# Kernel tuning notes

Hardware: AMD Instinct MI355X
Metric: run time of the kernel (lower is better)

## Reference

```python
import jax, jax.numpy as jnp
import numpy as np

D = 1024      # d_model
H = 16        # nhead
DH = D // H   # head_dim = 64
ROT = DH // 2 # rotary_ndims = 32
FFN = 4096    # d_ffn
B, T, M, N = 4, 1024, 128, 64


def _layernorm(x, g, b, eps=1e-5):
    mu = jnp.mean(x, axis=-1, keepdims=True)
    var = jnp.mean(jnp.square(x - mu), axis=-1, keepdims=True)
    return (x - mu) * jax.lax.rsqrt(var + eps) * g + b


def _rotate_half(x):
    x1, x2 = x[..., : x.shape[-1] // 2], x[..., x.shape[-1] // 2:]
    return jnp.concatenate([-x2, x1], axis=-1)


def setup_inputs() -> dict:
    key = jax.random.key(0)
    ks = jax.random.split(key, 16)
    s = 0.02
    inp = {
        'x': jax.random.normal(ks[0], (B, T, D), jnp.float32),
        'memory': jax.random.normal(ks[1], (B, M, D), jnp.float32),
        'nmr': jax.random.normal(ks[2], (B, N, D), jnp.float32),
        'Wq': jax.random.normal(ks[3], (D, D), jnp.float32) * s,
        'bq': jnp.zeros((D,), jnp.float32),
        'Wk': jax.random.normal(ks[4], (D, D), jnp.float32) * s,
        'bk': jnp.zeros((D,), jnp.float32),
        'Wv': jax.random.normal(ks[5], (D, D), jnp.float32) * s,
        'bv': jnp.zeros((D,), jnp.float32),
        'Wo': jax.random.normal(ks[6], (D, D), jnp.float32) * s,
        'bo': jnp.zeros((D,), jnp.float32),
        'W1': jax.random.normal(ks[7], (D, FFN), jnp.float32) * s,
        'b1': jnp.zeros((FFN,), jnp.float32),
        'W2': jax.random.normal(ks[8], (FFN, D), jnp.float32) * s,
        'b2': jnp.zeros((D,), jnp.float32),
        'ln1_g': jnp.ones((D,), jnp.float32),
        'ln1_b': jnp.zeros((D,), jnp.float32),
        'ln2_g': jnp.ones((D,), jnp.float32),
        'ln2_b': jnp.zeros((D,), jnp.float32),
    }
    return inp


def reference(x, memory, nmr, Wq, bq, Wk, bk, Wv, bv, Wo, bo, W1, b1, W2, b2,
              ln1_g, ln1_b, ln2_g, ln2_b):
    b, t, _ = x.shape
    m, n = memory.shape[1], nmr.shape[1]
    pref = m + n
    L = pref + t

    x_full = jnp.concatenate([memory, nmr, x], axis=1)  # (B, L, D)
    xa = _layernorm(x_full, ln1_g, ln1_b)

    def heads(w, bias):
        return (xa @ w + bias).reshape(b, L, H, DH).transpose(0, 2, 1, 3)  # (B,H,L,DH)

    q = heads(Wq, bq)
    k = heads(Wk, bk)
    v = heads(Wv, bv)

    # partial RoPE on first ROT dims of each head
    pos = jnp.arange(L, dtype=jnp.float32)
    inv_freq = 1.0 / (10000.0 ** (jnp.arange(0, ROT, 2, dtype=jnp.float32) / ROT))
    freqs = pos[:, None] * inv_freq[None, :]              # (L, ROT/2)
    emb = jnp.concatenate([freqs, freqs], axis=-1)        # (L, ROT)
    cos, sin = jnp.cos(emb), jnp.sin(emb)
    qr, qp = q[..., :ROT], q[..., ROT:]
    kr, kp = k[..., :ROT], k[..., ROT:]
    qr = qr * cos + _rotate_half(qr) * sin
    kr = kr * cos + _rotate_half(kr) * sin
    q = jnp.concatenate([qr, qp], axis=-1)
    k = jnp.concatenate([kr, kp], axis=-1)

    # block mask: prefix (memory+nmr) fully bidirectional, target causal,
    # target attends to full prefix, prefix does NOT attend to target.
    i = jnp.arange(L)
    allowed = (i[None, :] < pref) | ((i[:, None] >= pref) & (i[None, :] >= pref)
                                     & (i[None, :] <= i[:, None]))  # (L, L)

    scale = 1.0 / jnp.sqrt(jnp.asarray(DH, jnp.float32))
    scores = jnp.einsum('bhqd,bhkd->bhqk', q, k) * scale
    scores = jnp.where(allowed[None, None], scores, jnp.finfo(scores.dtype).min)
    probs = jax.nn.softmax(scores, axis=-1)
    attn = jnp.einsum('bhqk,bhkd->bhqd', probs, v)        # (B,H,L,DH)
    attn = attn.transpose(0, 2, 1, 3).reshape(b, L, D)

    x_full = attn @ Wo + bo + x_full

    xf = _layernorm(x_full, ln2_g, ln2_b)
    xf = jnp.square(jax.nn.relu(xf @ W1 + b1)) @ W2 + b2
    x_full = x_full + xf

    return x_full[:, pref:]
```

## Files before the change

### kernel.cpp

```cpp
#include <hip/hip_runtime.h>
#include <hip/hip_bf16.h>
#include <math.h>

#define D_   1024
#define H_   16
#define DH_  64
#define FFN_ 4096
#define B_   4
#define T_   1024
#define M_   128
#define N_   64
#define PREF 192
#define L_   1216
#define BL_  (B_*L_)
#define BT_  (B_*T_)

typedef __attribute__((ext_vector_type(4))) float f32x4;
typedef __attribute__((ext_vector_type(8))) short bf16x8;
typedef __attribute__((ext_vector_type(8))) unsigned short u16x8;
typedef const __attribute__((address_space(1))) void gvoid_t;
typedef __attribute__((address_space(3))) void lvoid_t;

#define LGKM0 asm volatile("s_waitcnt lgkmcnt(0)" ::: "memory")
#define CFENCE asm volatile("" ::: "memory")

__device__ __forceinline__ void gl_lds16(const void* g, void* l) {
    __builtin_amdgcn_global_load_lds((gvoid_t*)g, (lvoid_t*)l, 16, 0, 0);
}

__device__ __forceinline__ ushort f2bf(float x) {
    union { __hip_bfloat16 h; ushort u; } cv;
    cv.h = __float2bfloat16(x);
    return cv.u;
}

__device__ __forceinline__ u16x8 pack8(float4 a, float4 b) {
    u16x8 r;
    r[0]=f2bf(a.x); r[1]=f2bf(a.y); r[2]=f2bf(a.z); r[3]=f2bf(a.w);
    r[4]=f2bf(b.x); r[5]=f2bf(b.y); r[6]=f2bf(b.z); r[7]=f2bf(b.w);
    return r;
}

__device__ __forceinline__ float block_reduce_sum256(float v, float* sbuf) {
#pragma unroll
    for (int o = 32; o > 0; o >>= 1) v += __shfl_xor(v, o, 64);
    int w = threadIdx.x >> 6;
    if ((threadIdx.x & 63) == 0) sbuf[w] = v;
    __syncthreads();
    float r = sbuf[0] + sbuf[1] + sbuf[2] + sbuf[3];
    __syncthreads();
    return r;
}

__device__ __forceinline__ void wtr_body(const float* __restrict__ W,
                                         ushort* __restrict__ Wt, int K, int Nc)
{
    __shared__ float tl[64][65];
    int c0 = blockIdx.x << 6, k0 = blockIdx.y << 6;
    int tid = threadIdx.x;
    int rr = tid >> 4, c4 = (tid & 15) << 2;
#pragma unroll
    for (int p = 0; p < 4; ++p) {
        int r = (p << 4) + rr;
        float4 v = *(const float4*)(W + (size_t)(k0 + r) * Nc + c0 + c4);
        tl[r][c4+0] = v.x; tl[r][c4+1] = v.y; tl[r][c4+2] = v.z; tl[r][c4+3] = v.w;
    }
    __syncthreads();
#pragma unroll
    for (int p = 0; p < 4; ++p) {
        int rT = (p << 4) + rr;
        ushort4 uv;
        uv.x = f2bf(tl[c4+0][rT]);
        uv.y = f2bf(tl[c4+1][rT]);
        uv.z = f2bf(tl[c4+2][rT]);
        uv.w = f2bf(tl[c4+3][rT]);
        *(ushort4*)(Wt + (size_t)(c0 + rT) * K + k0 + c4) = uv;
    }
}

__global__ __launch_bounds__(256) void wtr_kernel(
    const float* __restrict__ W, ushort* __restrict__ Wt, int K, int Nc)
{ wtr_body(W, Wt, K, Nc); }

__global__ __launch_bounds__(256) void wtr4_kernel(
    const float* __restrict__ W0, const float* __restrict__ W1,
    const float* __restrict__ W2, const float* __restrict__ W3,
    ushort* __restrict__ T0, ushort* __restrict__ T1,
    ushort* __restrict__ T2, ushort* __restrict__ T3)
{
    const float* W; ushort* T;
    switch (blockIdx.z) {
        case 0: W = W0; T = T0; break;
        case 1: W = W1; T = T1; break;
        case 2: W = W2; T = T2; break;
        default: W = W3; T = T3; break;
    }
    wtr_body(W, T, D_, D_);
}

__global__ __launch_bounds__(256) void prep_kernel(
    float* __restrict__ tab, const float* __restrict__ bq,
    const float* __restrict__ bk, const float* __restrict__ bv,
    float* __restrict__ ob)
{
    int i = blockIdx.x * 256 + threadIdx.x;
    if (i < L_ * 32) {
        int pos = i >> 5, idx = i & 31;
        int fi = idx & 15;
        float invf = exp2f(-(float)fi * 0.83048202372f);
        float th = (float)pos * invf;
        tab[i] = (idx < 16) ? cosf(th) : sinf(th);
    } else {
        int j = i - L_ * 32;
        if (j < 3072) {
            float v = (j < 1024) ? bq[j] : (j < 2048 ? bk[j - 1024] : bv[j - 2048]);
            ob[j] = v;
        }
    }
}

__global__ __launch_bounds__(256) void ln1_concat_kernel(
    const float* __restrict__ x, const float* __restrict__ mem,
    const float* __restrict__ nmr, const float* __restrict__ g,
    const float* __restrict__ be, float* __restrict__ x_full,
    ushort* __restrict__ xa_bf)
{
    __shared__ float sbuf[4];
    int row = blockIdx.x;
    int b = row / L_, pos = row % L_;
    const float* src;
    if (pos < M_)          src = mem + ((size_t)b*M_ + pos)      * D_;
    else if (pos < M_+N_)  src = nmr + ((size_t)b*N_ + (pos-M_)) * D_;
    else                   src = x   + ((size_t)b*T_ + (pos-PREF))*D_;

    int c = threadIdx.x << 2;
    float4 v = *(const float4*)(src + c);
    float s = v.x + v.y + v.z + v.w;
    s = block_reduce_sum256(s, sbuf);
    float mu = s * (1.0f / D_);
    float dx = v.x - mu, dy = v.y - mu, dz = v.z - mu, dw = v.w - mu;
    float q = dx*dx + dy*dy + dz*dz + dw*dw;
    q = block_reduce_sum256(q, sbuf);
    float inv = rsqrtf(q * (1.0f / D_) + 1e-5f);
    float4 gv = *(const float4*)(g + c);
    float4 bv = *(const float4*)(be + c);
    ushort4 o;
    o.x = f2bf(dx*inv*gv.x + bv.x);
    o.y = f2bf(dy*inv*gv.y + bv.y);
    o.z = f2bf(dz*inv*gv.z + bv.z);
    o.w = f2bf(dw*inv*gv.w + bv.w);
    *(float4*)(x_full + (size_t)row*D_ + c) = v;
    *(ushort4*)(xa_bf + (size_t)row*D_ + c) = o;
}

__global__ __launch_bounds__(256) void ln2_kernel(
    const float* __restrict__ src, const float* __restrict__ g,
    const float* __restrict__ be, ushort* __restrict__ dst)
{
    __shared__ float sbuf[4];
    int row = blockIdx.x;
    int c = threadIdx.x << 2;
    float4 v = *(const float4*)(src + (size_t)row*D_ + c);
    float s = v.x + v.y + v.z + v.w;
    s = block_reduce_sum256(s, sbuf);
    float mu = s * (1.0f / D_);
    float dx = v.x - mu, dy = v.y - mu, dz = v.z - mu, dw = v.w - mu;
    float q = dx*dx + dy*dy + dz*dz + dw*dw;
    q = block_reduce_sum256(q, sbuf);
    float inv = rsqrtf(q * (1.0f / D_) + 1e-5f);
    float4 gv = *(const float4*)(g + c);
    float4 bv = *(const float4*)(be + c);
    ushort4 o;
    o.x = f2bf(dx*inv*gv.x + bv.x);
    o.y = f2bf(dy*inv*gv.y + bv.y);
    o.z = f2bf(dz*inv*gv.z + bv.z);
    o.w = f2bf(dw*inv*gv.w + bv.w);
    *(ushort4*)(dst + (size_t)row*D_ + c) = o;
}

__global__ __launch_bounds__(256) void gemm_bf16_kernel(
    const ushort* __restrict__ A, const ushort* __restrict__ Bt,
    const float* __restrict__ bias, const float* __restrict__ rtab,
    void* __restrict__ Cout, int Nc, int Kstride, int Klen, int mode)
{
    __shared__ ushort SM[24576];
    char* SMb = (char*)SM;
    int tid = threadIdx.x;
    int lane = tid & 63, w = tid >> 6;
    int wm = w >> 1, wn = w & 1;
    int nx = gridDim.x;
    int flat = blockIdx.y * nx + blockIdx.x;
    int cpx = (nx * gridDim.y) >> 3;
    int sz = (flat & 7) * cpx + (flat >> 3);
    int row0 = (sz / nx) << 7, col0 = (sz % nx) << 7;
    int l15 = lane & 15, l4 = lane >> 4;

    f32x4 acc[4][4] = {};

    int r_a = tid >> 2;
    int sc  = tid & 3;
    int lcOff = (sc ^ ((r_a >> 1) & 3)) << 3;
    const ushort* Arow  = A  + (size_t)(row0 + r_a)      * Kstride;
    const ushort* Arow2 = A  + (size_t)(row0 + 64 + r_a) * Kstride;
    const ushort* Brow  = Bt + (size_t)(col0 + r_a)      * Kstride;
    const ushort* Brow2 = Bt + (size_t)(col0 + 64 + r_a) * Kstride;

#define STAGEQ(bb, k0rel)                                                    \
    do { char* Ab = SMb + (bb)*8192; char* Bb = SMb + 24576 + (bb)*8192;     \
        gl_lds16(Arow  + (k0rel) + lcOff, Ab + (tid << 4));                  \
        gl_lds16(Arow2 + (k0rel) + lcOff, Ab + 4096 + (tid << 4));           \
        gl_lds16(Brow  + (k0rel) + lcOff, Bb + (tid << 4));                  \
        gl_lds16(Brow2 + (k0rel) + lcOff, Bb + 4096 + (tid << 4));           \
    } while (0)

    int nIt = Klen >> 5;
    STAGEQ(0, 0);
    STAGEQ(1, 32);
    int cur = 0;
    for (int it = 0; it < nIt; ++it) {
        if (it + 1 < nIt) {
            asm volatile("s_waitcnt vmcnt(4)" ::: "memory");
        } else {
            asm volatile("s_waitcnt vmcnt(0)" ::: "memory");
        }
        __builtin_amdgcn_s_barrier();
        CFENCE;
        if (it + 2 < nIt) {
            int s2 = cur + 2; if (s2 >= 3) s2 -= 3;
            STAGEQ(s2, (it + 2) << 5);
        }
        const ushort* As = (const ushort*)(SMb + cur*8192);
        const ushort* Bs = (const ushort*)(SMb + 24576 + cur*8192);
        bf16x8 af[4], bfr[4];
#pragma unroll
        for (int i = 0; i < 4; ++i) {
            int ra = (wm << 6) + (i << 4) + l15;
            af[i]  = *(const bf16x8*)(&As[ra*32 + ((l4 ^ ((ra >> 1) & 3)) << 3)]);
            int rb = (wn << 6) + (i << 4) + l15;
            bfr[i] = *(const bf16x8*)(&Bs[rb*32 + ((l4 ^ ((rb >> 1) & 3)) << 3)]);
        }
#pragma unroll
        for (int i = 0; i < 4; ++i)
#pragma unroll
            for (int j = 0; j < 4; ++j)
                acc[i][j] = __builtin_amdgcn_mfma_f32_16x16x32_bf16(af[i], bfr[j], acc[i][j], 0, 0, 0);
        CFENCE;
        cur = (cur + 1 == 3) ? 0 : cur + 1;
    }
#undef STAGEQ
    __syncthreads();

    float bcol[4];
#pragma unroll
    for (int j = 0; j < 4; ++j) bcol[j] = bias[col0 + (wn << 6) + (j << 4) + l15];

    float* scr = (float*)SM + w * 1088;
    int rr = lane >> 2, cseg = lane & 3;
    int hh = ((col0 & 1023) + (wn << 6)) >> 6;
    int which = col0 >> 10;

#pragma unroll
    for (int i = 0; i < 4; ++i) {
        LGKM0;
#pragma unroll
        for (int j = 0; j < 4; ++j)
#pragma unroll
            for (int r = 0; r < 4; ++r)
                scr[((l4 << 2) + r)*68 + (j << 4) + l15] = acc[i][j][r] + bcol[j];
        LGKM0;
        int grow = row0 + (wm << 6) + (i << 4) + rr;

        if (which == 2) {
            int r0g = row0 + (wm << 6) + (i << 4);
            int bb = r0g / L_;
            int posb = r0g - bb * L_;
            float4 v0, v1, v2, v3;
            v0.x = scr[ 0*68 + lane]; v0.y = scr[ 1*68 + lane];
            v0.z = scr[ 2*68 + lane]; v0.w = scr[ 3*68 + lane];
            v1.x = scr[ 4*68 + lane]; v1.y = scr[ 5*68 + lane];
            v1.z = scr[ 6*68 + lane]; v1.w = scr[ 7*68 + lane];
            v2.x = scr[ 8*68 + lane]; v2.y = scr[ 9*68 + lane];
            v2.z = scr[10*68 + lane]; v2.w = scr[11*68 + lane];
            v3.x = scr[12*68 + lane]; v3.y = scr[13*68 + lane];
            v3.z = scr[14*68 + lane]; v3.w = scr[15*68 + lane];
            ushort* O = (ushort*)Cout + 2*(size_t)BL_*D_;
            size_t base = ((size_t)(bb*H_ + hh)*64 + lane)*L_ + posb;
            *(u16x8*)(O + base)     = pack8(v0, v1);
            *(u16x8*)(O + base + 8) = pack8(v2, v3);
        } else {
            int bb = grow / L_;
            int pos = grow - bb * L_;
            float4 a0 = *(float4*)&scr[rr*68 + (cseg << 4) + 0];
            float4 a1 = *(float4*)&scr[rr*68 + (cseg << 4) + 4];
            float4 a2 = *(float4*)&scr[rr*68 + (cseg << 4) + 8];
            float4 a3 = *(float4*)&scr[rr*68 + (cseg << 4) + 12];
            if (cseg < 2) {
                int oseg = cseg ^ 1;
                float4 p0 = *(float4*)&scr[rr*68 + (oseg << 4) + 0];
                float4 p1 = *(float4*)&scr[rr*68 + (oseg << 4) + 4];
                float4 p2 = *(float4*)&scr[rr*68 + (oseg << 4) + 8];
                float4 p3 = *(float4*)&scr[rr*68 + (oseg << 4) + 12];
                const float* tb = rtab + pos*32;
                float4 c0 = *(const float4*)(tb + 0),  c1 = *(const float4*)(tb + 4);
                float4 c2 = *(const float4*)(tb + 8),  c3 = *(const float4*)(tb + 12);
                float4 s0 = *(const float4*)(tb + 16), s1 = *(const float4*)(tb + 20);
                float4 s2 = *(const float4*)(tb + 24), s3 = *(const float4*)(tb + 28);
                float sg = (cseg == 0) ? -1.f : 1.f;
                a0.x = a0.x*c0.x + sg*p0.x*s0.x; a0.y = a0.y*c0.y + sg*p0.y*s0.y;
                a0.z = a0.z*c0.z + sg*p0.z*s0.z; a0.w = a0.w*c0.w + sg*p0.w*s0.w;
                a1.x = a1.x*c1.x + sg*p1.x*s1.x; a1.y = a1.y*c1.y + sg*p1.y*s1.y;
                a1.z = a1.z*c1.z + sg*p1.z*s1.z; a1.w = a1.w*c1.w + sg*p1.w*s1.w;
                a2.x = a2.x*c2.x + sg*p2.x*s2.x; a2.y = a2.y*c2.y + sg*p2.y*s2.y;
                a2.z = a2.z*c2.z + sg*p2.z*s2.z; a2.w = a2.w*c2.w + sg*p2.w*s2.w;
                a3.x = a3.x*c3.x + sg*p3.x*s3.x; a3.y = a3.y*c3.y + sg*p3.y*s3.y;
                a3.z = a3.z*c3.z + sg*p3.z*s3.z; a3.w = a3.w*c3.w + sg*p3.w*s3.w;
            }
            ushort* O = (ushort*)Cout + (size_t)which * ((size_t)BL_*D_);
            size_t base = (((size_t)(bb*H_ + hh)*L_ + pos) << 6) + (cseg << 4);
            *(u16x8*)(O + base)     = pack8(a0, a1);
            *(u16x8*)(O + base + 8) = pack8(a2, a3);
        }
    }
}

__global__ __launch_bounds__(512) void gemm_ffn1_kernel(
    const ushort* __restrict__ A, const ushort* __restrict__ Bt,
    const float* __restrict__ bias, void* __restrict__ Cout,
    int Nc, int Kstride, int Klen)
{
    __shared__ ushort SM[36864];
    char* SMb = (char*)SM;

    int tid = threadIdx.x;
    int lane = tid & 63, w = tid >> 6;
    int l15 = lane & 15, l4 = lane >> 4;

    int nx = gridDim.x;
    int flat = blockIdx.y * nx + blockIdx.x;
    int cpx = (nx * gridDim.y) >> 3;
    int sz = (flat & 7) * cpx + (flat >> 3);
    int row0 = (sz / nx) << 7, col0 = (sz % nx) << 8;

    int wm = w >> 2, wn = w & 3;

    f32x4 acc[4][4] = {};

    int rA = tid >> 2, scA = tid & 3;
    int lcA = (scA ^ ((rA >> 1) & 3)) << 3;
    const ushort* Ar = A + (size_t)(row0 + rA) * Kstride + lcA;
    int lcB1 = (scA ^ (((128 + rA) >> 1) & 3)) << 3;
    const ushort* Br0 = Bt + (size_t)(col0 + rA)       * Kstride + lcA;
    const ushort* Br1 = Bt + (size_t)(col0 + 128 + rA) * Kstride + lcB1;

#define STG1(bb, k0rel)                                                       \
    do {                                                                      \
        gl_lds16(Ar  + (k0rel), SMb + (bb)*8192 + (tid << 4));                \
        gl_lds16(Br0 + (k0rel), SMb + 24576 + (bb)*16384 + (tid << 4));       \
        gl_lds16(Br1 + (k0rel), SMb + 24576 + (bb)*16384 + 8192 + (tid << 4));\
    } while (0)

    int nIt = Klen >> 5;
    STG1(0, 0);
    STG1(1, 32);
    int cur = 0;
    for (int it = 0; it < nIt; ++it) {
        if (it + 1 < nIt) {
            asm volatile("s_waitcnt vmcnt(3)" ::: "memory");
        } else {
            asm volatile("s_waitcnt vmcnt(0)" ::: "memory");
        }
        __builtin_amdgcn_s_barrier();
        CFENCE;
        if (it + 2 < nIt) {
            int s2 = cur + 2; if (s2 >= 3) s2 -= 3;
            STG1(s2, (it + 2) << 5);
        }
        const ushort* As = (const ushort*)(SMb + cur*8192);
        const ushort* Bs = (const ushort*)(SMb + 24576 + cur*16384);
        bf16x8 af[4], bfr[4];
#pragma unroll
        for (int i = 0; i < 4; ++i) {
            int ra = (wm << 6) + (i << 4) + l15;
            af[i]  = *(const bf16x8*)(&As[ra*32 + ((l4 ^ ((ra >> 1) & 3)) << 3)]);
            int rb = (wn << 6) + (i << 4) + l15;
            bfr[i] = *(const bf16x8*)(&Bs[rb*32 + ((l4 ^ ((rb >> 1) & 3)) << 3)]);
        }
#pragma unroll
        for (int i = 0; i < 4; ++i)
#pragma unroll
            for (int j = 0; j < 4; ++j)
                acc[i][j] = __builtin_amdgcn_mfma_f32_16x16x32_bf16(af[i], bfr[j], acc[i][j], 0, 0, 0);
        CFENCE;
        cur = (cur + 1 == 3) ? 0 : cur + 1;
    }
#undef STG1
    __syncthreads();

    float bcol[4];
#pragma unroll
    for (int j = 0; j < 4; ++j) bcol[j] = bias[col0 + (wn << 6) + (j << 4) + l15];

    float* scr = (float*)SMb + w * 1088;
    int rr = lane >> 2, cseg = lane & 3;
    int colbase = col0 + (wn << 6);

#pragma unroll
    for (int i = 0; i < 4; ++i) {
        LGKM0;
#pragma unroll
        for (int j = 0; j < 4; ++j)
#pragma unroll
            for (int r = 0; r < 4; ++r) {
                float v = acc[i][j][r] + bcol[j];
                v = fmaxf(v, 0.f); v *= v;
                scr[((l4 << 2) + r)*68 + (j << 4) + l15] = v;
            }
        LGKM0;
        int grow = row0 + (wm << 6) + (i << 4) + rr;
        float4 q0 = *(float4*)&scr[rr*68 + (cseg << 4) + 0];
        float4 q1 = *(float4*)&scr[rr*68 + (cseg << 4) + 4];
        float4 q2 = *(float4*)&scr[rr*68 + (cseg << 4) + 8];
        float4 q3 = *(float4*)&scr[rr*68 + (cseg << 4) + 12];
        int gcol = colbase + (cseg << 4);
        ushort* O = (ushort*)Cout;
        *(u16x8*)(O + (size_t)grow*Nc + gcol)     = pack8(q0, q1);
        *(u16x8*)(O + (size_t)grow*Nc + gcol + 8) = pack8(q2, q3);
    }
}

__global__ __launch_bounds__(256) void gemm_sk2_kernel(
    const ushort* __restrict__ A, const ushort* __restrict__ Bt,
    const float* __restrict__ bias, const float* __restrict__ res,
    float* __restrict__ Cout, int Nc, int Kstride, int Klen, int mode)
{
    __shared__ ushort SM[36864];
    char* SMb = (char*)SM;
    int tid = threadIdx.x;
    int lane = tid & 63, w = tid >> 6;
    int l15 = lane & 15, l4 = lane >> 4;
    int g = w >> 1, wm = w & 1;

    int nx = gridDim.x;
    int flat = blockIdx.y * nx + blockIdx.x;
    int cpx = (nx * gridDim.y) >> 3;
    int sz = (flat & 7) * cpx + (flat >> 3);
    int row0 = (sz / nx) << 7, col0 = (sz % nx) << 6;

    f32x4 acc[4][4] = {};
    const int kl = Klen >> 1;
    const int kb = g * kl;

    int gt = tid & 127;
    int rB = gt >> 2, sc = gt & 3;
    const ushort* Abase = A  + (size_t)row0 * Kstride + kb;
    const ushort* Bbase = Bt + (size_t)col0 * Kstride + kb;
    char* ALg = SMb + g * 24576;
    char* BLg = SMb + 49152 + g * 12288;

#define STG2(bb, k0rel)                                                       \
    do {                                                                      \
        _Pragma("unroll")                                                     \
        for (int p = 0; p < 4; ++p) {                                         \
            int rw = (p << 5) + rB; int lc = sc ^ ((rw >> 1) & 3);            \
            gl_lds16(Abase + (size_t)rw*Kstride + (k0rel) + (lc << 3),        \
                     ALg + (bb)*8192 + (p << 11) + (gt << 4));                \
        }                                                                     \
        _Pragma("unroll")                                                     \
        for (int p = 0; p < 2; ++p) {                                         \
            int rw = (p << 5) + rB; int lc = sc ^ ((rw >> 1) & 3);            \
            gl_lds16(Bbase + (size_t)rw*Kstride + (k0rel) + (lc << 3),        \
                     BLg + (bb)*4096 + (p << 11) + (gt << 4));                \
        }                                                                     \
    } while (0)

    int nIt = kl >> 5;
    STG2(0, 0);
    STG2(1, 32);
    int cur = 0;
    for (int it = 0; it < nIt; ++it) {
        if (it + 1 < nIt) {
            asm volatile("s_waitcnt vmcnt(6)" ::: "memory");
        } else {
            asm volatile("s_waitcnt vmcnt(0)" ::: "memory");
        }
        __builtin_amdgcn_s_barrier();
        CFENCE;
        if (it + 2 < nIt) {
            int s2 = cur + 2; if (s2 >= 3) s2 -= 3;
            STG2(s2, (it + 2) << 5);
        }
        const ushort* As = (const ushort*)(ALg + cur*8192);
        const ushort* Bs = (const ushort*)(BLg + cur*4096);
        bf16x8 af[4], bfr[4];
#pragma unroll
        for (int i = 0; i < 4; ++i) {
            int ra = (wm << 6) + (i << 4) + l15;
            af[i]  = *(const bf16x8*)(&As[ra*32 + ((l4 ^ ((ra >> 1) & 3)) << 3)]);
            int rb = (i << 4) + l15;
            bfr[i] = *(const bf16x8*)(&Bs[rb*32 + ((l4 ^ ((rb >> 1) & 3)) << 3)]);
        }
#pragma unroll
        for (int i = 0; i < 4; ++i)
#pragma unroll
            for (int j = 0; j < 4; ++j)
                acc[i][j] = __builtin_amdgcn_mfma_f32_16x16x32_bf16(af[i], bfr[j], acc[i][j], 0, 0, 0);
        CFENCE;
        cur = (cur + 1 == 3) ? 0 : cur + 1;
    }
#undef STG2
    __syncthreads();

    float* scr2 = (float*)SMb;
    if (g == 1) {
#pragma unroll
        for (int i = 0; i < 4; ++i)
#pragma unroll
            for (int j = 0; j < 4; ++j)
#pragma unroll
                for (int r = 0; r < 4; ++r)
                    scr2[((wm << 6) + (i << 4) + (l4 << 2) + r)*68 + (j << 4) + l15] = acc[i][j][r];
    }
    __syncthreads();
    if (g == 1) return;
#pragma unroll
    for (int i = 0; i < 4; ++i)
#pragma unroll
        for (int j = 0; j < 4; ++j)
#pragma unroll
            for (int r = 0; r < 4; ++r)
                acc[i][j][r] += scr2[((wm << 6) + (i << 4) + (l4 << 2) + r)*68 + (j << 4) + l15];

    float bcol[4];
#pragma unroll
    for (int j = 0; j < 4; ++j) bcol[j] = bias[col0 + (j << 4) + l15];
    int rr = lane >> 2, cseg = lane & 3;
    float* scr = (float*)(SMb + 36864) + w * 1088;

#pragma unroll
    for (int i = 0; i < 4; ++i) {
        LGKM0;
#pragma unroll
        for (int j = 0; j < 4; ++j)
#pragma unroll
            for (int r = 0; r < 4; ++r)
                scr[((l4 << 2) + r)*68 + (j << 4) + l15] = acc[i][j][r] + bcol[j];
        LGKM0;
        int grow = row0 + (wm << 6) + (i << 4) + rr;
        float4 q0 = *(float4*)&scr[rr*68 + (cseg << 4) + 0];
        float4 q1 = *(float4*)&scr[rr*68 + (cseg << 4) + 4];
        float4 q2 = *(float4*)&scr[rr*68 + (cseg << 4) + 8];
        float4 q3 = *(float4*)&scr[rr*68 + (cseg << 4) + 12];
        int gcol = col0 + (cseg << 4);
        size_t roff;
        if (mode == 2) {
            int rs = (grow >> 10)*L_ + PREF + (grow & (T_-1));
            roff = (size_t)rs*D_ + gcol;
        } else {
            roff = (size_t)grow*Nc + gcol;
        }
        float4 r0 = *(const float4*)(res + roff);
        float4 r1 = *(const float4*)(res + roff + 4);
        float4 r2 = *(const float4*)(res + roff + 8);
        float4 r3 = *(const float4*)(res + roff + 12);
        q0.x += r0.x; q0.y += r0.y; q0.z += r0.z; q0.w += r0.w;
        q1.x += r1.x; q1.y += r1.y; q1.z += r1.z; q1.w += r1.w;
        q2.x += r2.x; q2.y += r2.y; q2.z += r2.z; q2.w += r2.w;
        q3.x += r3.x; q3.y += r3.y; q3.z += r3.z; q3.w += r3.w;
        size_t o = (size_t)grow*Nc + gcol;
        *(float4*)(Cout + o)      = q0;
        *(float4*)(Cout + o + 4)  = q1;
        *(float4*)(Cout + o + 8)  = q2;
        *(float4*)(Cout + o + 12) = q3;
    }
}

__global__ __launch_bounds__(256) void attn_mfma_kernel(
    const ushort* __restrict__ qhd, const ushort* __restrict__ khd,
    const ushort* __restrict__ vt, ushort* __restrict__ attn_bf)
{
    __shared__ ushort Ks[2][64*64];
    __shared__ ushort Vs[2][64*64];
    __shared__ ushort Ps[4*16*64];

    int bid0 = blockIdx.x;
    int bid = (bid0 & 7) * (gridDim.x >> 3) + (bid0 >> 3);
    int p  = bid & 7;
    int h  = (bid >> 3) & (H_ - 1);
    int b  = bid >> 7;
    int tid = threadIdx.x, lane = tid & 63, w = tid >> 6;
    int l15 = lane & 15, lg = lane >> 4;
    int wq0 = w << 4;
    size_t bh = (size_t)(b * H_ + h);

    int srow = tid >> 3;
    int sslot = tid & 7;
    ushort* Ps_w = Ps + (w << 10);
    const float SC = 0.125f * 1.4426950408889634f;

#define STAGE_T(buf, t)                                                     \
    do { int j0s = (t) << 6;                                                \
        gl_lds16(khd + (bh * L_ + j0s + srow) * 64 + ((sslot ^ (srow & 7)) << 3),      \
                 (char*)Ks[buf] + (tid << 4));                              \
        gl_lds16(khd + (bh * L_ + j0s + 32 + srow) * 64 + ((sslot ^ ((32+srow) & 7)) << 3), \
                 (char*)Ks[buf] + ((256 + tid) << 4));                      \
        gl_lds16(vt + (bh * 64 + srow) * L_ + j0s + ((sslot ^ (srow & 7)) << 3),       \
                 (char*)Vs[buf] + (tid << 4));                              \
        gl_lds16(vt + (bh * 64 + 32 + srow) * L_ + j0s + ((sslot ^ ((32+srow) & 7)) << 3), \
                 (char*)Vs[buf] + ((256 + tid) << 4));                      \
    } while (0)

#pragma unroll
    for (int sub = 0; sub < 2; ++sub) {
        int qb = sub ? p : (15 - p);
        int i0 = PREF + (qb << 6);
        const ushort* qrow = qhd + (bh * L_ + i0 + wq0 + l15) * 64;
        bf16x8 bq0 = *(const bf16x8*)(qrow + (lg << 3));
        bf16x8 bq1 = *(const bf16x8*)(qrow + 32 + (lg << 3));

        f32x4 acc[4] = {};
        float mrun = -INFINITY;
        float lsum = 0.f;
        int qcap = i0 + wq0 + l15;

        int ntile = 4 + qb;
        STAGE_T(0, 0);
        __syncthreads();
        int cur = 0;
        for (int t = 0; t < ntile; ++t) {
            if (t + 1 < ntile) STAGE_T(cur ^ 1, t + 1);
            const ushort* Kc = Ks[cur];
            const ushort* Vc = Vs[cur];

            f32x4 s4[4];
            __builtin_amdgcn_s_setprio(1);
#pragma unroll
            for (int st = 0; st < 4; ++st) {
                int rk = (st << 4) + l15;
                bf16x8 ak0 = *(const bf16x8*)(Kc + (rk << 6) + ((lg       ^ (rk & 7)) << 3));
                bf16x8 ak1 = *(const bf16x8*)(Kc + (rk << 6) + (((4 + lg) ^ (rk & 7)) << 3));
                f32x4 z = {};
                z = __builtin_amdgcn_mfma_f32_16x16x32_bf16(ak0, bq0, z, 0, 0, 0);
                z = __builtin_amdgcn_mfma_f32_16x16x32_bf16(ak1, bq1, z, 0, 0, 0);
                s4[st] = z;
            }
            __builtin_amdgcn_s_setprio(0);

            int j0 = t << 6;
            float sv[4][4];
            bool diag = (t == ntile - 1);
            int kbq = j0 + (lg << 2);
#pragma unroll
            for (int st = 0; st < 4; ++st)
#pragma unroll
                for (int r = 0; r < 4; ++r) {
                    float s = s4[st][r] * SC;
                    if (diag && (kbq + (st << 4) + r > qcap)) s = -INFINITY;
                    sv[st][r] = s;
                }
            float bm;
            {
                float t0 = fmaxf(fmaxf(sv[0][0], sv[0][1]), fmaxf(sv[0][2], sv[0][3]));
                float t1 = fmaxf(fmaxf(sv[1][0], sv[1][1]), fmaxf(sv[1][2], sv[1][3]));
                float t2 = fmaxf(fmaxf(sv[2][0], sv[2][1]), fmaxf(sv[2][2], sv[2][3]));
                float t3 = fmaxf(fmaxf(sv[3][0], sv[3][1]), fmaxf(sv[3][2], sv[3][3]));
                bm = fmaxf(fmaxf(t0, t1), fmaxf(t2, t3));
            }
            bm = fmaxf(bm, __shfl_xor(bm, 16, 64));
            bm = fmaxf(bm, __shfl_xor(bm, 32, 64));

            float mn = fmaxf(mrun, bm);
            float cr = exp2f(mrun - mn);
            mrun = mn;
            float pe[4][4];
            float ps = 0.f;
#pragma unroll
            for (int st = 0; st < 4; ++st)
#pragma unroll
                for (int r = 0; r < 4; ++r) {
                    float e = exp2f(sv[st][r] - mn);
                    pe[st][r] = e; ps += e;
                }
            ps += __shfl_xor(ps, 16, 64);
            ps += __shfl_xor(ps, 32, 64);
            lsum = lsum * cr + ps;
#pragma unroll
            for (int su = 0; su < 4; ++su) acc[su] *= cr;

#pragma unroll
            for (int st = 0; st < 4; ++st) {
                int slot = (st << 1) + (lg >> 1);
                int sb = ((lg & 1) << 3);
#pragma unroll
                for (int rp = 0; rp < 2; ++rp) {
                    uint u = (uint)f2bf(pe[st][2*rp]) | ((uint)f2bf(pe[st][2*rp+1]) << 16);
                    *(uint*)((char*)Ps_w + l15*128 + ((slot ^ (l15 & 7)) << 4) + sb + (rp << 2)) = u;
                }
            }
            {
                bf16x8 bp0 = *(const bf16x8*)((char*)Ps_w + l15*128 + ((lg       ^ (l15 & 7)) << 4));
                bf16x8 bp1 = *(const bf16x8*)((char*)Ps_w + l15*128 + (((4 + lg) ^ (l15 & 7)) << 4));
                __builtin_amdgcn_s_setprio(1);
#pragma unroll
                for (int su = 0; su < 4; ++su) {
                    int rd = (su << 4) + l15;
                    bf16x8 av0 = *(const bf16x8*)(Vc + (rd << 6) + ((lg       ^ (rd & 7)) << 3));
                    bf16x8 av1 = *(const bf16x8*)(Vc + (rd << 6) + (((4 + lg) ^ (rd & 7)) << 3));
                    acc[su] = __builtin_amdgcn_mfma_f32_16x16x32_bf16(av0, bp0, acc[su], 0, 0, 0);
                    acc[su] = __builtin_amdgcn_mfma_f32_16x16x32_bf16(av1, bp1, acc[su], 0, 0, 0);
                }
                __builtin_amdgcn_s_setprio(0);
            }
            __syncthreads();
            cur ^= 1;
        }

        float rl = 1.0f / lsum;
        size_t orow = (size_t)b * T_ + (i0 - PREF) + wq0 + l15;
#pragma unroll
        for (int su = 0; su < 4; ++su) {
            ushort4 o4;
            o4.x = f2bf(acc[su][0] * rl);
            o4.y = f2bf(acc[su][1] * rl);
            o4.z = f2bf(acc[su][2] * rl);
            o4.w = f2bf(acc[su][3] * rl);
            *(ushort4*)(attn_bf + orow * D_ + (h << 6) + (su << 4) + (lg << 2)) = o4;
        }
        __syncthreads();
    }
#undef STAGE_T
}

extern "C" void kernel_launch(void* const* d_in, const int* in_sizes, int n_in,
                              void* d_out, int out_size, void* d_ws, size_t ws_size,
                              hipStream_t stream) {
    const float* x   = (const float*)d_in[0];
    const float* mem = (const float*)d_in[1];
    const float* nmr = (const float*)d_in[2];
    const float* Wq  = (const float*)d_in[3];
    const float* bq  = (const float*)d_in[4];
    const float* Wk  = (const float*)d_in[5];
    const float* bk  = (const float*)d_in[6];
    const float* Wv  = (const float*)d_in[7];
    const float* bv  = (const float*)d_in[8];
    const float* Wo  = (const float*)d_in[9];
    const float* bo  = (const float*)d_in[10];
    const float* W1  = (const float*)d_in[11];
    const float* b1  = (const float*)d_in[12];
    const float* W2  = (const float*)d_in[13];
    const float* b2  = (const float*)d_in[14];
    const float* g1  = (const float*)d_in[15];
    const float* be1 = (const float*)d_in[16];
    const float* g2  = (const float*)d_in[17];
    const float* be2 = (const float*)d_in[18];
    float* out = (float*)d_out;

    const size_t BLD = (size_t)BL_ * D_;
    const size_t BTD = (size_t)BT_ * D_;

    float* f = (float*)d_ws;
    float* x_full = f;
    float* x2     = f + BLD;
    float* bqkv   = x2 + BTD;
    float* rtab   = bqkv + 4096;
    ushort* bfb   = (ushort*)(rtab + (size_t)L_*32);
    ushort* xa_bf   = bfb;
    ushort* qhd     = bfb + BLD;
    ushort* khd     = bfb + 2*BLD;
    ushort* vt      = bfb + 3*BLD;
    ushort* h1_bf   = bfb + 4*BLD;
    ushort* wq_bf = h1_bf + (size_t)BT_*FFN_;
    ushort* wk_bf = wq_bf + (size_t)D_*D_;
    ushort* wv_bf = wk_bf + (size_t)D_*D_;
    ushort* wo_bf = wv_bf + (size_t)D_*D_;
    ushort* w1_bf = wo_bf + (size_t)D_*D_;
    ushort* w2_bf = w1_bf + (size_t)D_*FFN_;
    ushort* attn_bf = xa_bf;
    ushort* ln2_bf  = qhd;

    wtr4_kernel<<<dim3(16, 16, 4), 256, 0, stream>>>(Wq, Wk, Wv, Wo,
                                                     wq_bf, wk_bf, wv_bf, wo_bf);
    wtr_kernel<<<dim3(FFN_/64, D_/64),   256, 0, stream>>>(W1, w1_bf, D_,   FFN_);
    wtr_kernel<<<dim3(D_/64,   FFN_/64), 256, 0, stream>>>(W2, w2_bf, FFN_, D_);
    prep_kernel<<<(L_*32 + 3072 + 255)/256, 256, 0, stream>>>(rtab, bq, bk, bv, bqkv);

    ln1_concat_kernel<<<BL_, 256, 0, stream>>>(x, mem, nmr, g1, be1, x_full, xa_bf);

    gemm_bf16_kernel<<<dim3(3072/128, BL_/128), 256, 0, stream>>>(
        xa_bf, wq_bf, bqkv, rtab, qhd, D_, D_, D_, 7);

    attn_mfma_kernel<<<B_*H_*8, 256, 0, stream>>>(qhd, khd, vt, attn_bf);

    gemm_sk2_kernel<<<dim3(D_/64, BT_/128), 256, 0, stream>>>(
        attn_bf, wo_bf, bo, x_full, x2, D_, D_, D_, 2);

    ln2_kernel<<<BT_, 256, 0, stream>>>(x2, g2, be2, ln2_bf);

    gemm_ffn1_kernel<<<dim3(FFN_/256, BT_/128), 512, 0, stream>>>(
        ln2_bf, w1_bf, b1, h1_bf, FFN_, D_, D_);

    gemm_sk2_kernel<<<dim3(D_/64, BT_/128), 256, 0, stream>>>(
        h1_bf, w2_bf, b2, x2, out, D_, FFN_, FFN_, 1);
}
```

Baseline: 238.4 us.

## Split-K FFN2 GEMM over wide-tile kernel with separate reduction pass

Turns the FFN1 GEMM kernel into a template. The second FFN matmul now reuses it with 128x256 tiles and a 4-way split of K across blockIdx.z, writing fp32 partial sums to a workspace. A new reduce kernel sums the four partials and adds the bias and residual. This replaces the 64-column sk2 kernel, aiming for larger tiles with more reuse while keeping enough blocks in the grid, at the cost of extra fp32 partial traffic and one more launch. It also assumes the workspace has room for 64MB of partials.

```diff
diff --git a/kernel.cpp b/kernel.cpp
--- a/kernel.cpp
+++ b/kernel.cpp
@@ -176,6 +176,28 @@
     o.z = f2bf(dz*inv*gv.z + bv.z);
     o.w = f2bf(dw*inv*gv.w + bv.w);
     *(ushort4*)(dst + (size_t)row*D_ + c) = o;
+}
+
+__global__ __launch_bounds__(256) void reduce4_out_kernel(
+    const float* __restrict__ part, const float* __restrict__ b2,
+    const float* __restrict__ x2, float* __restrict__ out)
+{
+    int row = blockIdx.x;
+    int c = threadIdx.x << 2;
+    size_t o = (size_t)row * D_ + c;
+    const size_t S = (size_t)BT_ * D_;
+    float4 p0 = *(const float4*)(part + o);
+    float4 p1 = *(const float4*)(part + S + o);
+    float4 p2 = *(const float4*)(part + 2*S + o);
+    float4 p3 = *(const float4*)(part + 3*S + o);
+    float4 bb = *(const float4*)(b2 + c);
+    float4 rv = *(const float4*)(x2 + o);
+    float4 v;
+    v.x = p0.x + p1.x + p2.x + p3.x + bb.x + rv.x;
+    v.y = p0.y + p1.y + p2.y + p3.y + bb.y + rv.y;
+    v.z = p0.z + p1.z + p2.z + p3.z + bb.z + rv.z;
+    v.w = p0.w + p1.w + p2.w + p3.w + bb.w + rv.w;
+    *(float4*)(out + o) = v;
 }
 
 __global__ __launch_bounds__(256) void gemm_bf16_kernel(
@@ -323,7 +345,8 @@
     }
 }
 
-__global__ __launch_bounds__(512) void gemm_ffn1_kernel(
+template<int MODE>
+__global__ __launch_bounds__(512) void gemm_wide_kernel(
     const ushort* __restrict__ A, const ushort* __restrict__ Bt,
     const float* __restrict__ bias, void* __restrict__ Cout,
     int Nc, int Kstride, int Klen)
@@ -340,6 +363,7 @@
     int cpx = (nx * gridDim.y) >> 3;
     int sz = (flat & 7) * cpx + (flat >> 3);
     int row0 = (sz / nx) << 7, col0 = (sz % nx) << 8;
+    int kbase = blockIdx.z * Klen;
 
     int wm = w >> 2, wn = w & 3;
 
@@ -347,10 +371,10 @@
 
     int rA = tid >> 2, scA = tid & 3;
     int lcA = (scA ^ ((rA >> 1) & 3)) << 3;
-    const ushort* Ar = A + (size_t)(row0 + rA) * Kstride + lcA;
+    const ushort* Ar = A + (size_t)(row0 + rA) * Kstride + kbase + lcA;
     int lcB1 = (scA ^ (((128 + rA) >> 1) & 3)) << 3;
-    const ushort* Br0 = Bt + (size_t)(col0 + rA)       * Kstride + lcA;
-    const ushort* Br1 = Bt + (size_t)(col0 + 128 + rA) * Kstride + lcB1;
+    const ushort* Br0 = Bt + (size_t)(col0 + rA)       * Kstride + kbase + lcA;
+    const ushort* Br1 = Bt + (size_t)(col0 + 128 + rA) * Kstride + kbase + lcB1;
 
 #define STG1(bb, k0rel)                                                       \
     do {                                                                      \
@@ -396,9 +420,11 @@
 #undef STG1
     __syncthreads();
 
-    float bcol[4];
-#pragma unroll
-    for (int j = 0; j < 4; ++j) bcol[j] = bias[col0 + (wn << 6) + (j << 4) + l15];
+    float bcol[4] = {0.f, 0.f, 0.f, 0.f};
+    if (MODE != 4) {
+#pragma unroll
+        for (int j = 0; j < 4; ++j) bcol[j] = bias[col0 + (wn << 6) + (j << 4) + l15];
+    }
 
     float* scr = (float*)SMb + w * 1088;
     int rr = lane >> 2, cseg = lane & 3;
@@ -412,7 +438,7 @@
 #pragma unroll
             for (int r = 0; r < 4; ++r) {
                 float v = acc[i][j][r] + bcol[j];
-                v = fmaxf(v, 0.f); v *= v;
+                if (MODE == 3) { v = fmaxf(v, 0.f); v *= v; }
                 scr[((l4 << 2) + r)*68 + (j << 4) + l15] = v;
             }
         LGKM0;
@@ -422,9 +448,18 @@
         float4 q2 = *(float4*)&scr[rr*68 + (cseg << 4) + 8];
         float4 q3 = *(float4*)&scr[rr*68 + (cseg << 4) + 12];
         int gcol = colbase + (cseg << 4);
-        ushort* O = (ushort*)Cout;
-        *(u16x8*)(O + (size_t)grow*Nc + gcol)     = pack8(q0, q1);
-        *(u16x8*)(O + (size_t)grow*Nc + gcol + 8) = pack8(q2, q3);
+        if (MODE == 3) {
+            ushort* O = (ushort*)Cout;
+            *(u16x8*)(O + (size_t)grow*Nc + gcol)     = pack8(q0, q1);
+            *(u16x8*)(O + (size_t)grow*Nc + gcol + 8) = pack8(q2, q3);
+        } else {
+            float* O = (float*)Cout + (size_t)blockIdx.z * ((size_t)BT_ * D_);
+            size_t o = (size_t)grow*Nc + gcol;
+            *(float4*)(O + o)      = q0;
+            *(float4*)(O + o + 4)  = q1;
+            *(float4*)(O + o + 8)  = q2;
+            *(float4*)(O + o + 12) = q3;
+        }
     }
 }
 
@@ -774,6 +809,7 @@
     ushort* wo_bf = wv_bf + (size_t)D_*D_;
     ushort* w1_bf = wo_bf + (size_t)D_*D_;
     ushort* w2_bf = w1_bf + (size_t)D_*FFN_;
+    float* partials = (float*)(w2_bf + (size_t)FFN_*D_);
     ushort* attn_bf = xa_bf;
     ushort* ln2_bf  = qhd;
 
@@ -795,9 +831,10 @@
 
     ln2_kernel<<<BT_, 256, 0, stream>>>(x2, g2, be2, ln2_bf);
 
-    gemm_ffn1_kernel<<<dim3(FFN_/256, BT_/128), 512, 0, stream>>>(
+    gemm_wide_kernel<3><<<dim3(FFN_/256, BT_/128), 512, 0, stream>>>(
         ln2_bf, w1_bf, b1, h1_bf, FFN_, D_, D_);
 
-    gemm_sk2_kernel<<<dim3(D_/64, BT_/128), 256, 0, stream>>>(
-        h1_bf, w2_bf, b2, x2, out, D_, FFN_, FFN_, 1);
-}
+    gemm_wide_kernel<4><<<dim3(D_/256, BT_/128, 4), 512, 0, stream>>>(
+        h1_bf, w2_bf, nullptr, partials, D_, FFN_, FFN_/4);
+    reduce4_out_kernel<<<BT_, 256, 0, stream>>>(partials, b2, x2, out);
+}
```

Result: slower. 251.8 us (+5.6%).
